# Performance work log

Hardware: AMD Instinct MI355X
Metric: run time of the kernel (lower is better)

The kernel has to match this reference:

```python
import jax, jax.numpy as jnp
import numpy as np

B, IN, H = 8192, 512, 512


def _binarize(w):
    # sign() forward with straight-through gradient (ebnn Binarize)
    return w + jax.lax.stop_gradient(jnp.sign(w) - w)


def setup_inputs() -> dict:
    key = jax.random.key(0)
    ks = jax.random.split(key, 7)
    stdv = 1.0 / np.sqrt(H)
    return {
        "x": jax.random.normal(ks[0], (B, IN), jnp.float32),
        "hx": jax.random.normal(ks[1], (B, H), jnp.float32),
        "cx": jax.random.normal(ks[2], (B, H), jnp.float32),
        "W_ih": jax.random.uniform(ks[3], (4 * H, IN), jnp.float32, -stdv, stdv),
        "W_hh": jax.random.uniform(ks[4], (4 * H, H), jnp.float32, -stdv, stdv),
        "bias_ih": jax.random.uniform(ks[5], (4 * H,), jnp.float32, -stdv, stdv),
        "bias_hh": jax.random.uniform(ks[6], (4 * H,), jnp.float32, -stdv, stdv),
    }


def reference(x, hx, cx, W_ih, W_hh, bias_ih, bias_hh):
    # gates: [B, 4H] = x @ sign(W_ih)^T + b_ih + hx @ sign(W_hh)^T + b_hh
    gates = (jnp.einsum("bi,gi->bg", x, _binarize(W_ih)) + bias_ih
             + jnp.einsum("bh,gh->bg", hx, _binarize(W_hh)) + bias_hh)
    ingate, forgetgate, cellgate, outgate = jnp.split(gates, 4, axis=1)
    cy = jax.nn.sigmoid(forgetgate) * cx + jax.nn.sigmoid(ingate) * jnp.tanh(cellgate)
    hy = jax.nn.sigmoid(outgate) * jnp.tanh(cy)
    return (hy, cy)
```

## Files before the change

### kernel.cpp

```cpp
#include <hip/hip_runtime.h>
#include <hip/hip_bf16.h>
#include <stdint.h>


typedef __attribute__((ext_vector_type(4))) int int4x;
typedef __attribute__((ext_vector_type(4))) float float4x;

#define B_DIM 8192
#define H_DIM 512

__device__ __forceinline__ float bf2f(uint16_t u) {
  return __uint_as_float(((uint32_t)u) << 16);
}
__device__ __forceinline__ uint16_t f2bf(float f) {
  uint32_t u = __float_as_uint(f);
  return (uint16_t)((u + 0x7FFFu + ((u >> 16) & 1u)) >> 16);
}
__device__ __forceinline__ float sigm(float x) { return 1.0f / (1.0f + __expf(-x)); }
__device__ __forceinline__ float tanh_f(float x) { return 2.0f / (1.0f + __expf(-2.0f * x)) - 1.0f; }

__device__ __forceinline__ void gld_lds16(const void* g, void* l) {
  __builtin_amdgcn_global_load_lds((const __attribute__((address_space(1))) char*)g,
                                   (__attribute__((address_space(3))) char*)l, 16, 0, 0);
}

__device__ __forceinline__ int detect_f32(const void* x) {
  const int l = threadIdx.x & 63;
  uint32_t wrd = ((const uint32_t*)x)[l];
  uint32_t e0 = (wrd >> 7) & 0xFFu, e1 = (wrd >> 23) & 0xFFu;
  return __ballot(e0 > 0x85u || e1 > 0x85u) != 0ull;
}

__global__ __launch_bounds__(256) void prep_kernel(
    const void* __restrict__ x, const void* __restrict__ hx,
    const void* __restrict__ w_ih, const void* __restrict__ w_hh,
    int8_t* __restrict__ Xhi, int8_t* __restrict__ Xlo, int8_t* __restrict__ Bp) {
  const int isF32 = detect_f32(x);
  const long gtid = (long)blockIdx.x * 256 + threadIdx.x;
  if (gtid < 524288L) {
    const int tile = (int)(gtid >> 6);
    const int lane = (int)(gtid & 63);
    const int kt = tile & 15;
    const int m = ((tile >> 4) << 4) | (lane & 15);
    const int k = kt * 64 + (lane >> 4) * 16;
    const void* src = (k < 512) ? x : hx;
    const long soff = (long)m * 512 + (k & 511);
    float v[16];
    if (isF32) {
      const float4x* s4 = (const float4x*)((const float*)src + soff);
#pragma unroll
      for (int q = 0; q < 4; ++q) {
        float4x t = s4[q];
        v[q * 4] = t[0]; v[q * 4 + 1] = t[1]; v[q * 4 + 2] = t[2]; v[q * 4 + 3] = t[3];
      }
    } else {
      const uint16_t* s = (const uint16_t*)src + soff;
#pragma unroll
      for (int j = 0; j < 16; ++j) v[j] = bf2f(s[j]);
    }
    union { int8_t b[16]; int4x v4; } uh, ul;
#pragma unroll
    for (int j = 0; j < 16; ++j) {
      float c = fminf(fmaxf(v[j], -8.0f), 8.0f);
      int xf = __float2int_rn(c * 4096.0f);
      xf = xf > 32639 ? 32639 : xf;
      xf = xf < -32768 ? -32768 : xf;
      const int lo = (xf << 24) >> 24;
      const int hi = (xf - lo) >> 8;
      ul.b[j] = (int8_t)lo;
      uh.b[j] = (int8_t)hi;
    }
    *(int4x*)(Xhi + (long)tile * 1024 + lane * 16) = uh.v4;
    *(int4x*)(Xlo + (long)tile * 1024 + lane * 16) = ul.v4;
  } else {
    const long g2 = gtid - 524288L;
    const int tile = (int)(g2 >> 6);
    const int lane = (int)(g2 & 63);
    const int kt = tile & 15;
    const int p = ((tile >> 4) << 4) | (lane & 15);
    const int n = (p & 3) * 512 + (p >> 2);
    const int k = kt * 64 + (lane >> 4) * 16;
    const void* src = (k < 512) ? w_ih : w_hh;
    const long soff = (long)n * 512 + (k & 511);
    union { int8_t b[16]; int4x v4; } us;
    if (isF32) {
      const float4x* s4 = (const float4x*)((const float*)src + soff);
#pragma unroll
      for (int q = 0; q < 4; ++q) {
        float4x t = s4[q];
#pragma unroll
        for (int j = 0; j < 4; ++j) {
          const float wv = t[j];
          us.b[q * 4 + j] = (int8_t)(wv > 0.f ? 1 : (wv < 0.f ? -1 : 0));
        }
      }
    } else {
      const uint16_t* s = (const uint16_t*)src + soff;
#pragma unroll
      for (int j = 0; j < 16; ++j) {
        const uint16_t u = s[j];
        us.b[j] = (int8_t)(((u & 0x7FFFu) == 0) ? 0 : ((u & 0x8000u) ? -1 : 1));
      }
    }
    *(int4x*)(Bp + (long)tile * 1024 + lane * 16) = us.v4;
  }
}

__global__ __launch_bounds__(256, 4) void blstm_gemm_kernel(
    const int8_t* __restrict__ Xhi, const int8_t* __restrict__ Xlo,
    const int8_t* __restrict__ Bp, const void* __restrict__ b_ih,
    const void* __restrict__ b_hh, const void* __restrict__ cx,
    const void* __restrict__ xdet, void* __restrict__ out) {
  __shared__ alignas(16) char lds[20480];
  const int tid = threadIdx.x;
  const int l = tid & 63, w = tid >> 6;
  const int lrow = l & 15, lq = l >> 4;
  const int isF32 = detect_f32(xdet);
  const int bx = blockIdx.x, by = blockIdx.y;

  const int8_t* sp[5];
  int dof[5];
#pragma unroll
  for (int i = 0; i < 5; ++i) {
    const int c = w * 5 + i;
    if (c < 8) {
      sp[i] = Xhi + ((long)(by * 8 + c) * 16) * 1024 + l * 16;
      dof[i] = c * 1024;
    } else if (c < 16) {
      sp[i] = Xlo + ((long)(by * 8 + (c - 8)) * 16) * 1024 + l * 16;
      dof[i] = 8192 + (c - 8) * 1024;
    } else {
      sp[i] = Bp + ((long)(bx * 4 + (c - 16)) * 16) * 1024 + l * 16;
      dof[i] = 16384 + (c - 16) * 1024;
    }
  }

  int4x acch[2][4], accl[2][4];
#pragma unroll
  for (int mt = 0; mt < 2; ++mt)
#pragma unroll
    for (int nt = 0; nt < 4; ++nt) {
      acch[mt][nt] = (int4x){0, 0, 0, 0};
      accl[mt][nt] = (int4x){0, 0, 0, 0};
    }

  for (int ks = 0; ks < 16; ++ks) {
    __syncthreads();
#pragma unroll
    for (int i = 0; i < 5; ++i) {
      gld_lds16(sp[i], lds + dof[i]);
      sp[i] += 1024;
    }
    __syncthreads();
    int4x ah[2], al[2], b[4];
#pragma unroll
    for (int mt = 0; mt < 2; ++mt) {
      ah[mt] = *(const int4x*)(lds + (w * 2 + mt) * 1024 + l * 16);
      al[mt] = *(const int4x*)(lds + 8192 + (w * 2 + mt) * 1024 + l * 16);
    }
#pragma unroll
    for (int nt = 0; nt < 4; ++nt)
      b[nt] = *(const int4x*)(lds + 16384 + nt * 1024 + l * 16);
#pragma unroll
    for (int mt = 0; mt < 2; ++mt)
#pragma unroll
      for (int nt = 0; nt < 4; ++nt) {
        acch[mt][nt] = __builtin_amdgcn_mfma_i32_16x16x64_i8(ah[mt], b[nt], acch[mt][nt], 0, 0, 0);
        accl[mt][nt] = __builtin_amdgcn_mfma_i32_16x16x64_i8(al[mt], b[nt], accl[mt][nt], 0, 0, 0);
      }
  }

  const long CYo = (long)B_DIM * H_DIM;
  float biasv[4];
#pragma unroll
  for (int nt = 0; nt < 4; ++nt) {
    const int c = bx * 16 + nt * 4 + (lrow >> 2);
    const int n = (l & 3) * 512 + c;
    if (isF32)
      biasv[nt] = ((const float*)b_ih)[n] + ((const float*)b_hh)[n];
    else
      biasv[nt] = bf2f(((const uint16_t*)b_ih)[n]) + bf2f(((const uint16_t*)b_hh)[n]);
  }
  float* outF = (float*)out;
  uint16_t* outB = (uint16_t*)out;
  const int base = l & ~3;
#pragma unroll
  for (int mt = 0; mt < 2; ++mt) {
#pragma unroll
    for (int nt = 0; nt < 4; ++nt) {
      const int c = bx * 16 + nt * 4 + (lrow >> 2);
      const int rowbase = by * 128 + (w * 2 + mt) * 16 + lq * 4;
      float myi = 0.f, myf = 0.f, myg = 0.f, myo = 0.f;
#pragma unroll
      for (int r = 0; r < 4; ++r) {
        const float v = fmaf((float)acch[mt][nt][r], 0.0625f,
                             (float)accl[mt][nt][r] * (1.0f / 4096.0f)) + biasv[nt];
        const float vi = __shfl(v, base + 0, 64);
        const float vf = __shfl(v, base + 1, 64);
        const float vg = __shfl(v, base + 2, 64);
        const float vo = __shfl(v, base + 3, 64);
        if ((l & 3) == r) { myi = vi; myf = vf; myg = vg; myo = vo; }
      }
      const int row = rowbase + (l & 3);
      const long cidx = (long)row * H_DIM + c;
      const float cxv = isF32 ? ((const float*)cx)[cidx] : bf2f(((const uint16_t*)cx)[cidx]);
      const float ig = sigm(myi), fg = sigm(myf), og = sigm(myo);
      const float cg = tanh_f(myg);
      const float cy = fg * cxv + ig * cg;
      const float hy = og * tanh_f(cy);
      if (isF32) {
        outF[cidx] = hy;
        outF[CYo + cidx] = cy;
      } else {
        outB[cidx] = f2bf(hy);
        outB[CYo + cidx] = f2bf(cy);
      }
    }
  }
}

extern "C" void kernel_launch(void* const* d_in, const int* in_sizes, int n_in,
                              void* d_out, int out_size, void* d_ws, size_t ws_size,
                              hipStream_t stream) {
  const void* x = d_in[0];
  const void* hx = d_in[1];
  const void* cx = d_in[2];
  const void* W_ih = d_in[3];
  const void* W_hh = d_in[4];
  const void* b_ih = d_in[5];
  const void* b_hh = d_in[6];
  char* ws = (char*)d_ws;
  int8_t* Xhi = (int8_t*)ws;
  int8_t* Xlo = (int8_t*)(ws + 8388608);
  int8_t* Bp = (int8_t*)(ws + 16777216);

  prep_kernel<<<2560, 256, 0, stream>>>(x, hx, W_ih, W_hh, Xhi, Xlo, Bp);
  dim3 grid(32, 64);
  blstm_gemm_kernel<<<grid, 256, 0, stream>>>(Xhi, Xlo, Bp, b_ih, b_hh, cx, x, d_out);
}
```

Baseline: 160.0 us.

## Double-buffer LDS loads and relayout gate weights to drop epilogue shuffles

The GEMM main loop now uses two LDS buffers, so the global-to-LDS loads for the next k-step are issued before the MFMAs on the current step, and one barrier per iteration is removed. The prep kernel is reorganised so each wave reads a full contiguous input row. The weight permutation places the four gates of one hidden column in separate n-tiles, which lets the epilogue combine i/f/g/o directly from registers without cross-lane shuffles. The cost is double the LDS per block (40 KB), which may reduce occupancy below the requested 4 blocks per CU, and the prep writes are now scattered rather than contiguous.

Measured after the change: 166.5 us. 1.04x slower.

```diff
diff --git a/kernel.cpp b/kernel.cpp
--- a/kernel.cpp
+++ b/kernel.cpp
@@ -36,15 +36,13 @@
     const void* __restrict__ w_ih, const void* __restrict__ w_hh,
     int8_t* __restrict__ Xhi, int8_t* __restrict__ Xlo, int8_t* __restrict__ Bp) {
   const int isF32 = detect_f32(x);
-  const long gtid = (long)blockIdx.x * 256 + threadIdx.x;
-  if (gtid < 524288L) {
-    const int tile = (int)(gtid >> 6);
-    const int lane = (int)(gtid & 63);
-    const int kt = tile & 15;
-    const int m = ((tile >> 4) << 4) | (lane & 15);
-    const int k = kt * 64 + (lane >> 4) * 16;
-    const void* src = (k < 512) ? x : hx;
-    const long soff = (long)m * 512 + (k & 511);
+  const int w = threadIdx.x >> 6, l = threadIdx.x & 63;
+  const int half = l >> 5, lk = l & 31;
+  if (blockIdx.x < 2048) {
+    const int m = blockIdx.x * 4 + w;
+    const int k = half * 512 + lk * 16;
+    const void* src = half ? hx : x;
+    const long soff = (long)m * 512 + lk * 16;
     float v[16];
     if (isF32) {
       const float4x* s4 = (const float4x*)((const float*)src + soff);
@@ -70,18 +68,16 @@
       ul.b[j] = (int8_t)lo;
       uh.b[j] = (int8_t)hi;
     }
-    *(int4x*)(Xhi + (long)tile * 1024 + lane * 16) = uh.v4;
-    *(int4x*)(Xlo + (long)tile * 1024 + lane * 16) = ul.v4;
+    const int tile = ((m >> 4) << 4) | (k >> 6);
+    const int lit = ((l & 3) << 4) | (m & 15);
+    *(int4x*)(Xhi + (long)tile * 1024 + lit * 16) = uh.v4;
+    *(int4x*)(Xlo + (long)tile * 1024 + lit * 16) = ul.v4;
   } else {
-    const long g2 = gtid - 524288L;
-    const int tile = (int)(g2 >> 6);
-    const int lane = (int)(g2 & 63);
-    const int kt = tile & 15;
-    const int p = ((tile >> 4) << 4) | (lane & 15);
-    const int n = (p & 3) * 512 + (p >> 2);
-    const int k = kt * 64 + (lane >> 4) * 16;
-    const void* src = (k < 512) ? w_ih : w_hh;
-    const long soff = (long)n * 512 + (k & 511);
+    const int p = (blockIdx.x - 2048) * 4 + w;
+    const int n = ((p >> 4) & 3) * 512 + ((p >> 6) << 4) + (p & 15);
+    const int k = half * 512 + lk * 16;
+    const void* src = half ? w_hh : w_ih;
+    const long soff = (long)n * 512 + lk * 16;
     union { int8_t b[16]; int4x v4; } us;
     if (isF32) {
       const float4x* s4 = (const float4x*)((const float*)src + soff);
@@ -102,7 +98,9 @@
         us.b[j] = (int8_t)(((u & 0x7FFFu) == 0) ? 0 : ((u & 0x8000u) ? -1 : 1));
       }
     }
-    *(int4x*)(Bp + (long)tile * 1024 + lane * 16) = us.v4;
+    const int tile = ((p >> 4) << 4) | (k >> 6);
+    const int lit = ((l & 3) << 4) | (p & 15);
+    *(int4x*)(Bp + (long)tile * 1024 + lit * 16) = us.v4;
   }
 }
 
@@ -111,7 +109,7 @@
     const int8_t* __restrict__ Bp, const void* __restrict__ b_ih,
     const void* __restrict__ b_hh, const void* __restrict__ cx,
     const void* __restrict__ xdet, void* __restrict__ out) {
-  __shared__ alignas(16) char lds[20480];
+  __shared__ alignas(16) char lds[40960];
   const int tid = threadIdx.x;
   const int l = tid & 63, w = tid >> 6;
   const int lrow = l & 15, lq = l >> 4;
@@ -144,23 +142,32 @@
       accl[mt][nt] = (int4x){0, 0, 0, 0};
     }
 
+#pragma unroll
+  for (int i = 0; i < 5; ++i) {
+    gld_lds16(sp[i], lds + dof[i]);
+    sp[i] += 1024;
+  }
+
   for (int ks = 0; ks < 16; ++ks) {
     __syncthreads();
-#pragma unroll
-    for (int i = 0; i < 5; ++i) {
-      gld_lds16(sp[i], lds + dof[i]);
-      sp[i] += 1024;
-    }
-    __syncthreads();
+    const char* cur = lds + (ks & 1) * 20480;
+    if (ks < 15) {
+      char* nb = lds + ((ks + 1) & 1) * 20480;
+#pragma unroll
+      for (int i = 0; i < 5; ++i) {
+        gld_lds16(sp[i], nb + dof[i]);
+        sp[i] += 1024;
+      }
+    }
     int4x ah[2], al[2], b[4];
 #pragma unroll
     for (int mt = 0; mt < 2; ++mt) {
-      ah[mt] = *(const int4x*)(lds + (w * 2 + mt) * 1024 + l * 16);
-      al[mt] = *(const int4x*)(lds + 8192 + (w * 2 + mt) * 1024 + l * 16);
+      ah[mt] = *(const int4x*)(cur + (w * 2 + mt) * 1024 + l * 16);
+      al[mt] = *(const int4x*)(cur + 8192 + (w * 2 + mt) * 1024 + l * 16);
     }
 #pragma unroll
     for (int nt = 0; nt < 4; ++nt)
-      b[nt] = *(const int4x*)(lds + 16384 + nt * 1024 + l * 16);
+      b[nt] = *(const int4x*)(cur + 16384 + nt * 1024 + l * 16);
 #pragma unroll
     for (int mt = 0; mt < 2; ++mt)
 #pragma unroll
@@ -171,41 +178,31 @@
   }
 
   const long CYo = (long)B_DIM * H_DIM;
+  const int c = bx * 16 + lrow;
   float biasv[4];
 #pragma unroll
-  for (int nt = 0; nt < 4; ++nt) {
-    const int c = bx * 16 + nt * 4 + (lrow >> 2);
-    const int n = (l & 3) * 512 + c;
+  for (int g = 0; g < 4; ++g) {
     if (isF32)
-      biasv[nt] = ((const float*)b_ih)[n] + ((const float*)b_hh)[n];
+      biasv[g] = ((const float*)b_ih)[g * 512 + c] + ((const float*)b_hh)[g * 512 + c];
     else
-      biasv[nt] = bf2f(((const uint16_t*)b_ih)[n]) + bf2f(((const uint16_t*)b_hh)[n]);
+      biasv[g] = bf2f(((const uint16_t*)b_ih)[g * 512 + c]) + bf2f(((const uint16_t*)b_hh)[g * 512 + c]);
   }
   float* outF = (float*)out;
   uint16_t* outB = (uint16_t*)out;
-  const int base = l & ~3;
 #pragma unroll
   for (int mt = 0; mt < 2; ++mt) {
 #pragma unroll
-    for (int nt = 0; nt < 4; ++nt) {
-      const int c = bx * 16 + nt * 4 + (lrow >> 2);
-      const int rowbase = by * 128 + (w * 2 + mt) * 16 + lq * 4;
-      float myi = 0.f, myf = 0.f, myg = 0.f, myo = 0.f;
-#pragma unroll
-      for (int r = 0; r < 4; ++r) {
-        const float v = fmaf((float)acch[mt][nt][r], 0.0625f,
-                             (float)accl[mt][nt][r] * (1.0f / 4096.0f)) + biasv[nt];
-        const float vi = __shfl(v, base + 0, 64);
-        const float vf = __shfl(v, base + 1, 64);
-        const float vg = __shfl(v, base + 2, 64);
-        const float vo = __shfl(v, base + 3, 64);
-        if ((l & 3) == r) { myi = vi; myf = vf; myg = vg; myo = vo; }
-      }
-      const int row = rowbase + (l & 3);
+    for (int r = 0; r < 4; ++r) {
+      const int row = by * 128 + (w * 2 + mt) * 16 + lq * 4 + r;
       const long cidx = (long)row * H_DIM + c;
+      float vg[4];
+#pragma unroll
+      for (int g = 0; g < 4; ++g)
+        vg[g] = fmaf((float)acch[mt][g][r], 0.0625f,
+                     fmaf((float)accl[mt][g][r], 2.44140625e-4f, biasv[g]));
       const float cxv = isF32 ? ((const float*)cx)[cidx] : bf2f(((const uint16_t*)cx)[cidx]);
-      const float ig = sigm(myi), fg = sigm(myf), og = sigm(myo);
-      const float cg = tanh_f(myg);
+      const float ig = sigm(vg[0]), fg = sigm(vg[1]), og = sigm(vg[3]);
+      const float cg = tanh_f(vg[2]);
       const float cy = fg * cxv + ig * cg;
       const float hy = og * tanh_f(cy);
       if (isF32) {
```
